# Kernel tuning notes

Hardware: AMD Instinct MI355X
Metric: run time of the kernel (lower is better)

The kernel has to match this reference:

```python
import jax, jax.numpy as jnp
import numpy as np

B, N, H, S, C = 32, 64, 128, 100, 16
SIGMA = 0.5  # perturbations.perturbed default noise scale


def setup_inputs() -> dict:
    key = jax.random.key(0)
    ks = jax.random.split(key, 8)
    x = jax.random.normal(ks[0], (B, N, H), jnp.float32)
    a = (jax.random.uniform(ks[1], (B, N, N)) < 0.1).astype(jnp.float32)
    adj = jnp.maximum(a, jnp.swapaxes(a, -1, -2))  # symmetric binary adjacency
    counts = jax.random.randint(ks[2], (B,), N // 2, N + 1)
    mask = jnp.arange(N)[None, :] < counts[:, None]
    sc = 1.0 / np.sqrt(H).astype(np.float32)
    W1 = jax.random.normal(ks[3], (H, H), jnp.float32) * sc
    b1 = jnp.zeros((H,), jnp.float32)
    W2 = jax.random.normal(ks[4], (H, H), jnp.float32) * sc
    b2 = jnp.zeros((H,), jnp.float32)
    cW1 = jax.random.normal(ks[5], (H, H), jnp.float32) * sc
    cb1 = jnp.zeros((H,), jnp.float32)
    cW2 = jax.random.normal(ks[6], (H, C), jnp.float32) * sc
    cb2 = jnp.zeros((C,), jnp.float32)
    noise = jax.random.normal(ks[7], (S * B, N, H), jnp.float32)
    return dict(x=x, adj=adj, mask=mask, W1=W1, b1=b1, W2=W2, b2=b2,
                cW1=cW1, cb1=cb1, cW2=cW2, cb2=cb2, noise=noise, num_samples=S)


def _gcn(x, adj, mask, W, b):
    # DenseGCNConv: set diag to 1, symmetric-normalize, propagate, mask.
    h = x @ W
    n = adj.shape[-1]
    eye = jnp.eye(n, dtype=bool)
    a = jnp.where(eye, 1.0, adj)
    d = jnp.clip(a.sum(-1), 1.0, None) ** -0.5
    a = d[..., :, None] * a * d[..., None, :]
    out = a @ h + b
    return out * mask[..., None].astype(out.dtype)


def _perturbed_clustering(x_all, adj_all, mask_all, cW1, cb1, cW2, cb2):
    BS, n, h = x_all.shape
    # concept MLP + argmax
    logits = jax.nn.relu(x_all @ cW1 + cb1) @ cW2 + cb2
    concepts = jnp.argmax(logits, axis=-1)  # [BS, n]
    same = concepts[:, :, None] == concepts[:, None, :]
    adj_c = jnp.where(same, adj_all, 0.0)
    # connected components via min-label propagation (scipy-order relabel)
    edge = (adj_c > 0) & mask_all[:, :, None] & mask_all[:, None, :]
    labels0 = jnp.where(mask_all, jnp.arange(n, dtype=jnp.int32), n)

    def body(_, labels):
        neigh = jnp.min(jnp.where(edge, labels[:, None, :], n), axis=-1)
        return jnp.minimum(labels, neigh)

    roots = jax.lax.fori_loop(0, n, body, labels0)  # min node idx of component
    present = jnp.zeros((BS, n + 1), jnp.int32).at[
        jnp.arange(BS)[:, None], roots].max(mask_all.astype(jnp.int32))
    rank = jnp.cumsum(present[:, :n], axis=-1)  # 1-based compact id per root
    assignments = jnp.where(
        mask_all,
        jnp.take_along_axis(rank, jnp.minimum(roots, n - 1), axis=-1), 0)
    # scatter-reduce pooling; segment ids flatten (batch, cluster); slot 0 = masked
    seg = (jnp.arange(BS, dtype=jnp.int32)[:, None] * (n + 1) + assignments).reshape(-1)
    x_new = jax.ops.segment_sum(x_all.reshape(BS * n, h), seg,
                                num_segments=BS * (n + 1)).reshape(BS, n + 1, h)[:, 1:]
    row = jax.ops.segment_max(adj_all.reshape(BS * n, n), seg,
                              num_segments=BS * (n + 1)).reshape(BS, n + 1, n)[:, 1:]
    row = jnp.maximum(row, 0.0)  # torch_scatter max includes zero-init
    colsrc = jnp.swapaxes(row, 1, 2).reshape(BS * n, n)
    adj_new = jax.ops.segment_max(colsrc, seg,
                                  num_segments=BS * (n + 1)).reshape(BS, n + 1, n)[:, 1:]
    adj_new = jnp.maximum(jnp.swapaxes(adj_new, 1, 2), 0.0)
    num_clusters = jnp.max(assignments, axis=-1)
    mask_new = jnp.arange(n)[None, :] < num_clusters[:, None]
    return x_new, adj_new, mask_new, assignments


def reference(x, adj, mask, W1, b1, W2, b2, cW1, cb1, cW2, cb2, noise, num_samples):
    # embedding GCN stack
    xe = jax.nn.relu(_gcn(x, adj, mask, W1, b1))
    x_emb = jax.nn.relu(_gcn(xe, adj, mask, W2, b2))
    Bb, n, h = x_emb.shape
    # perturbed replication (sample-major layout, matching final reshape(S, -1, ...))
    adj_all = jnp.tile(adj, (num_samples, 1, 1))
    mask_all = jnp.tile(mask, (num_samples, 1))
    x_all = jnp.tile(x_emb, (num_samples, 1, 1)) + SIGMA * noise
    x_new, adj_new, mask_new, assignments = _perturbed_clustering(
        x_all, adj_all, mask_all, cW1, cb1, cW2, cb2)
    # perturbed expectation for x_new; explicit mean/max in forward for adj/mask
    x_new = x_new.reshape(num_samples, Bb, n, h).mean(axis=0)
    adj_new = adj_new.reshape(num_samples, Bb, n, n).mean(axis=0)
    mask_new = jnp.max(mask_new.reshape(num_samples, Bb, n), axis=0)
    return x_new, adj_new, assignments, x_emb, mask_new
```

## Files before the change

kernel.cpp:

```cpp
#include <hip/hip_runtime.h>
#include <cstdint>

#define B_ 32
#define N_ 64
#define H_ 128
#define S_ 100
#define C_ 16
#define SIGMA_ 0.5f

#define OFF_XNEW 0
#define OFF_ADJN 262144
#define OFF_ASGN 393216
#define OFF_XEMB 598016
#define OFF_MSKN 860160

__device__ __forceinline__ int read_mask_elem(const void* mp, int idx) {
    const unsigned int* u = (const unsigned int*)mp;
    const unsigned int w0 = u[0], w1 = u[1];
    if (w0 == 1u) {
        if (w1 == 1u) return ((const int*)mp)[idx] != 0;
        return ((const int*)mp)[2 * idx] != 0;
    }
    if (w0 == 0x3f800000u) return ((const float*)mp)[idx] != 0.0f;
    if (w0 == 0u) return ((const double*)mp)[idx] != 0.0;
    return ((const unsigned char*)mp)[idx] != 0;
}

__global__ __launch_bounds__(256) void gcn_kernel(
    const float* __restrict__ x, const float* __restrict__ adj,
    const void* __restrict__ maskp,
    const float* __restrict__ W1, const float* __restrict__ b1,
    const float* __restrict__ W2, const float* __restrict__ b2,
    float* __restrict__ out,
    unsigned long long* __restrict__ abits_ws,
    unsigned long long* __restrict__ mbits_ws)
{
    const int b = blockIdx.x;
    const int t = threadIdx.x;
    __shared__ float Xs[N_][130];
    __shared__ float Hs[N_][130];
    __shared__ float An[N_][65];
    __shared__ float dsh[N_];
    __shared__ unsigned long long mb_sh;

    if (t < 64) {
        const int mv = read_mask_elem(maskp, b * N_ + t);
        const unsigned long long bal = __ballot(mv != 0);
        if (t == 0) { mb_sh = bal; mbits_ws[b] = bal; }
    }
    for (int row = (t >> 6); row < N_; row += 4) {
        const int j = t & 63;
        const float v = adj[((size_t)b * N_ + row) * N_ + j];
        const unsigned long long bal = __ballot(v > 0.0f);
        if (j == 0) abits_ws[b * N_ + row] = bal;
        An[row][j] = (row == j) ? 1.0f : v;
    }
    __syncthreads();
    if (t < 64) {
        float s = 0.0f;
        for (int j = 0; j < N_; ++j) s += An[t][j];
        if (s < 1.0f) s = 1.0f;
        dsh[t] = 1.0f / sqrtf(s);
    }
    __syncthreads();
    for (int e = t; e < N_ * N_; e += 256) {
        const int i = e >> 6, j = e & 63;
        An[i][j] *= dsh[i] * dsh[j];
    }
    for (int e = t; e < N_ * H_; e += 256)
        Xs[e >> 7][e & 127] = x[(size_t)b * N_ * H_ + e];
    __syncthreads();

    const int ng = t & 15, kg = t >> 4;
    const unsigned long long mb = mb_sh;

    {
        float acc[4][8] = {};
        for (int d = 0; d < H_; ++d) {
            float xv[4];
#pragma unroll
            for (int r = 0; r < 4; ++r) xv[r] = Xs[4 * ng + r][d];
            const float4 wa = *(const float4*)(W1 + d * H_ + 8 * kg);
            const float4 wb = *(const float4*)(W1 + d * H_ + 8 * kg + 4);
            const float wf[8] = {wa.x, wa.y, wa.z, wa.w, wb.x, wb.y, wb.z, wb.w};
#pragma unroll
            for (int j = 0; j < 8; ++j)
#pragma unroll
                for (int r = 0; r < 4; ++r) acc[r][j] += xv[r] * wf[j];
        }
#pragma unroll
        for (int r = 0; r < 4; ++r)
#pragma unroll
            for (int j = 0; j < 8; ++j) Hs[4 * ng + r][8 * kg + j] = acc[r][j];
    }
    __syncthreads();
    {
        float acc[4][8] = {};
        for (int j2 = 0; j2 < N_; ++j2) {
            float av[4];
#pragma unroll
            for (int r = 0; r < 4; ++r) av[r] = An[4 * ng + r][j2];
            float hv[8];
#pragma unroll
            for (int j = 0; j < 8; ++j) hv[j] = Hs[j2][8 * kg + j];
#pragma unroll
            for (int j = 0; j < 8; ++j)
#pragma unroll
                for (int r = 0; r < 4; ++r) acc[r][j] += av[r] * hv[j];
        }
        const float4 ba = *(const float4*)(b1 + 8 * kg);
        const float4 bb = *(const float4*)(b1 + 8 * kg + 4);
        const float bf[8] = {ba.x, ba.y, ba.z, ba.w, bb.x, bb.y, bb.z, bb.w};
#pragma unroll
        for (int r = 0; r < 4; ++r) {
            const int i = 4 * ng + r;
            const float m = ((mb >> i) & 1ull) ? 1.0f : 0.0f;
#pragma unroll
            for (int j = 0; j < 8; ++j)
                Xs[i][8 * kg + j] = fmaxf(acc[r][j] + bf[j], 0.0f) * m;
        }
    }
    __syncthreads();
    {
        float acc[4][8] = {};
        for (int d = 0; d < H_; ++d) {
            float xv[4];
#pragma unroll
            for (int r = 0; r < 4; ++r) xv[r] = Xs[4 * ng + r][d];
            const float4 wa = *(const float4*)(W2 + d * H_ + 8 * kg);
            const float4 wb = *(const float4*)(W2 + d * H_ + 8 * kg + 4);
            const float wf[8] = {wa.x, wa.y, wa.z, wa.w, wb.x, wb.y, wb.z, wb.w};
#pragma unroll
            for (int j = 0; j < 8; ++j)
#pragma unroll
                for (int r = 0; r < 4; ++r) acc[r][j] += xv[r] * wf[j];
        }
        __syncthreads();
#pragma unroll
        for (int r = 0; r < 4; ++r)
#pragma unroll
            for (int j = 0; j < 8; ++j) Hs[4 * ng + r][8 * kg + j] = acc[r][j];
    }
    __syncthreads();
    {
        float acc[4][8] = {};
        for (int j2 = 0; j2 < N_; ++j2) {
            float av[4];
#pragma unroll
            for (int r = 0; r < 4; ++r) av[r] = An[4 * ng + r][j2];
            float hv[8];
#pragma unroll
            for (int j = 0; j < 8; ++j) hv[j] = Hs[j2][8 * kg + j];
#pragma unroll
            for (int j = 0; j < 8; ++j)
#pragma unroll
                for (int r = 0; r < 4; ++r) acc[r][j] += av[r] * hv[j];
        }
        const float4 ba = *(const float4*)(b2 + 8 * kg);
        const float4 bb = *(const float4*)(b2 + 8 * kg + 4);
        const float bf[8] = {ba.x, ba.y, ba.z, ba.w, bb.x, bb.y, bb.z, bb.w};
#pragma unroll
        for (int r = 0; r < 4; ++r) {
            const int i = 4 * ng + r;
            const float m = ((mb >> i) & 1ull) ? 1.0f : 0.0f;
#pragma unroll
            for (int j = 0; j < 8; ++j)
                out[OFF_XEMB + (size_t)b * N_ * H_ + i * H_ + 8 * kg + j] =
                    fmaxf(acc[r][j] + bf[j], 0.0f) * m;
        }
    }
}

__device__ __forceinline__ float rscat16(float* v, int kg) {
#pragma unroll
    for (int i = 0; i < 8; ++i) {
        const float send = (kg & 8) ? v[i] : v[i + 8];
        const float recv = __shfl_xor(send, 8);
        v[i] = ((kg & 8) ? v[i + 8] : v[i]) + recv;
    }
#pragma unroll
    for (int i = 0; i < 4; ++i) {
        const float send = (kg & 4) ? v[i] : v[i + 4];
        const float recv = __shfl_xor(send, 4);
        v[i] = ((kg & 4) ? v[i + 4] : v[i]) + recv;
    }
#pragma unroll
    for (int i = 0; i < 2; ++i) {
        const float send = (kg & 2) ? v[i] : v[i + 2];
        const float recv = __shfl_xor(send, 2);
        v[i] = ((kg & 2) ? v[i + 2] : v[i]) + recv;
    }
    {
        const float send = (kg & 1) ? v[0] : v[1];
        const float recv = __shfl_xor(send, 1);
        v[0] = ((kg & 1) ? v[1] : v[0]) + recv;
    }
    return v[0];
}

__device__ __forceinline__ void argmax16(float bv, int kg, int* dst) {
    int bi = kg;
#pragma unroll
    for (int m = 1; m <= 8; m <<= 1) {
        const float ov = __shfl_xor(bv, m);
        const int   oi = __shfl_xor(bi, m);
        if (ov > bv || (ov == bv && oi < bi)) { bv = ov; bi = oi; }
    }
    if (kg == 0) *dst = bi;
}

__global__ __launch_bounds__(256) void sample_kernel(
    const float* __restrict__ noise,
    const float* __restrict__ cW1, const float* __restrict__ cb1,
    const float* __restrict__ cW2, const float* __restrict__ cb2,
    const unsigned long long* __restrict__ abits_ws,
    const unsigned long long* __restrict__ mbits_ws,
    float* __restrict__ out, int* __restrict__ gNcl)
{
    const int sb = blockIdx.x;
    const int b  = sb & (B_ - 1);
    const int t  = threadIdx.x;
    __shared__ float xa[N_ * H_];
    __shared__ int   concepts[N_];
    __shared__ unsigned long long reachL[N_];
    __shared__ unsigned long long cmS[N_];
    __shared__ unsigned long long roS[N_];
    __shared__ unsigned long long abS[N_];
    __shared__ unsigned int presLo, presHi;

    const unsigned long long mb = mbits_ws[b];
    if (t < 64) abS[t] = abits_ws[b * N_ + t];
    if (t == 0) { presLo = 0u; presHi = 0u; }

    {
        const float4* e4 = (const float4*)(out + OFF_XEMB + (size_t)b * N_ * H_);
        const float4* n4 = (const float4*)(noise + (size_t)sb * N_ * H_);
        float4* x4 = (float4*)xa;
        for (int idx = t; idx < N_ * 32; idx += 256) {
            const int i = idx >> 5, cc = idx & 31;
            const float4 ev = e4[idx], nv = n4[idx];
            float4 v;
            v.x = ev.x + SIGMA_ * nv.x;  v.y = ev.y + SIGMA_ * nv.y;
            v.z = ev.z + SIGMA_ * nv.z;  v.w = ev.w + SIGMA_ * nv.w;
            x4[i * 32 + (cc ^ (i & 7))] = v;
        }
    }
    __syncthreads();

    const int ng = t >> 4, kg = t & 15;
    float acc[4][8] = {};
    {
        const float4* x4 = (const float4*)xa;
        const int swzb = 4 * (ng & 1);
        for (int cc = 0; cc < 32; ++cc) {
            float xv[4][4];
#pragma unroll
            for (int r = 0; r < 4; ++r) {
                const float4 tmp = x4[(4 * ng + r) * 32 + (cc ^ (swzb + r))];
                xv[r][0] = tmp.x; xv[r][1] = tmp.y; xv[r][2] = tmp.z; xv[r][3] = tmp.w;
            }
#pragma unroll
            for (int dd = 0; dd < 4; ++dd) {
                const int d = cc * 4 + dd;
                const float4 wa = *(const float4*)(cW1 + d * H_ + 8 * kg);
                const float4 wb = *(const float4*)(cW1 + d * H_ + 8 * kg + 4);
                const float wf[8] = {wa.x, wa.y, wa.z, wa.w, wb.x, wb.y, wb.z, wb.w};
#pragma unroll
                for (int j = 0; j < 8; ++j)
#pragma unroll
                    for (int r = 0; r < 4; ++r) acc[r][j] += xv[r][dd] * wf[j];
            }
        }
    }
    {
        const float4 ba = *(const float4*)(cb1 + 8 * kg);
        const float4 bb = *(const float4*)(cb1 + 8 * kg + 4);
        const float bf[8] = {ba.x, ba.y, ba.z, ba.w, bb.x, bb.y, bb.z, bb.w};
        const float cb2v = cb2[kg];
#pragma unroll
        for (int r = 0; r < 4; ++r) {
            float h[8];
#pragma unroll
            for (int j = 0; j < 8; ++j) h[j] = fmaxf(acc[r][j] + bf[j], 0.0f);
            float pl[16] = {};
#pragma unroll
            for (int j = 0; j < 8; ++j) {
                const float4* w2r = (const float4*)(cW2 + (8 * kg + j) * C_);
                const float4 w0 = w2r[0], w1 = w2r[1], w2v = w2r[2], w3 = w2r[3];
                const float wf2[16] = {w0.x, w0.y, w0.z, w0.w, w1.x, w1.y, w1.z, w1.w,
                                       w2v.x, w2v.y, w2v.z, w2v.w, w3.x, w3.y, w3.z, w3.w};
#pragma unroll
                for (int c = 0; c < C_; ++c) pl[c] += h[j] * wf2[c];
            }
            const float l = rscat16(pl, kg) + cb2v;
            argmax16(l, kg, &concepts[4 * ng + r]);
        }
    }
    __syncthreads();

    unsigned long long reach = 0ull;
    int masked_i = 0;
    if (t < 64) {
        masked_i = (int)((mb >> t) & 1ull);
        if (masked_i) {
            const int ci = concepts[t];
            unsigned long long mm = abS[t] & mb;
            unsigned long long em = 0ull;
            while (mm) {
                const int j = __builtin_ctzll(mm);
                if (concepts[j] == ci) em |= (1ull << j);
                mm &= mm - 1;
            }
            reach = em | (1ull << t);
        }
        reachL[t] = reach;
    }
    __syncthreads();
    for (;;) {
        unsigned long long r = reach;
        if (masked_i) {
            unsigned long long mm = reach & ~(1ull << t);
            while (mm) {
                const int j = __builtin_ctzll(mm);
                r |= reachL[j];
                mm &= mm - 1;
            }
        }
        const int changed = (r != reach);
        __syncthreads();
        if (t < 64) reachL[t] = r;
        reach = r;
        if (!__syncthreads_or(changed)) break;
    }
    int root = 0;
    if (masked_i) {
        root = __builtin_ctzll(reach);
        if (root < 32) atomicOr(&presLo, 1u << root);
        else           atomicOr(&presHi, 1u << (root - 32));
    }
    __syncthreads();
    const unsigned long long present =
        ((unsigned long long)presHi << 32) | (unsigned long long)presLo;
    const int ncl = __popcll(present);
    if (t < 64) {
        int a_i = 0;
        if (masked_i) {
            a_i = __popcll(present & ((1ull << root) - 1ull)) + 1;
            if (root == t) {
                cmS[a_i - 1] = reach;
                unsigned long long ro = 0ull, mm = reach;
                while (mm) { const int j = __builtin_ctzll(mm); ro |= abS[j]; mm &= mm - 1; }
                roS[a_i - 1] = ro;
            }
        }
        out[OFF_ASGN + (size_t)sb * N_ + t] = (float)a_i;
    }
    __syncthreads();

    for (int e = t; e < ncl * H_; e += 256) {
        const int c = e >> 7, d = e & 127;
        unsigned long long mm = cmS[c];
        float s = 0.0f;
        while (mm) {
            const int j = __builtin_ctzll(mm);
            s += xa[j * H_ + ((((d >> 2) ^ (j & 7)) << 2) | (d & 3))];
            mm &= mm - 1;
        }
        atomicAdd(&out[OFF_XNEW + (size_t)b * N_ * H_ + e], s);
    }
    {
        int* adjCnt = (int*)out + OFF_ADJN;
        for (int idx = t; idx < ncl * N_; idx += 256) {
            const int c1 = idx >> 6, c2 = idx & 63;
            if (c2 < ncl && (roS[c1] & cmS[c2]))
                atomicAdd(&adjCnt[b * N_ * N_ + idx], 1);
        }
    }
    if (t == 0) atomicMax(&gNcl[b], ncl);
}

__global__ __launch_bounds__(256) void finalize_kernel(
    float* __restrict__ out, const int* __restrict__ gNcl)
{
    const int idx = blockIdx.x * 256 + threadIdx.x;
    if (idx < OFF_ADJN) {
        out[idx] = out[idx] / 100.0f;
    } else if (idx < OFF_ASGN) {
        const int c = ((const int*)out)[idx];
        out[idx] = (float)c / 100.0f;
    } else {
        const int m = idx - OFF_ASGN;
        if (m < B_ * N_) {
            const int bb = m >> 6, k = m & 63;
            out[OFF_MSKN + m] = (k < gNcl[bb]) ? 1.0f : 0.0f;
        }
    }
}

extern "C" void kernel_launch(void* const* d_in, const int* in_sizes, int n_in,
                              void* d_out, int out_size, void* d_ws, size_t ws_size,
                              hipStream_t stream) {
    (void)in_sizes; (void)n_in; (void)out_size; (void)ws_size;
    const float* x    = (const float*)d_in[0];
    const float* adj  = (const float*)d_in[1];
    const void*  mskp = d_in[2];
    const float* W1   = (const float*)d_in[3];
    const float* b1   = (const float*)d_in[4];
    const float* W2   = (const float*)d_in[5];
    const float* b2   = (const float*)d_in[6];
    const float* cW1  = (const float*)d_in[7];
    const float* cb1  = (const float*)d_in[8];
    const float* cW2  = (const float*)d_in[9];
    const float* cb2  = (const float*)d_in[10];
    const float* noise = (const float*)d_in[11];
    float* out = (float*)d_out;

    int* gNcl = (int*)d_ws;
    unsigned long long* abits_ws = (unsigned long long*)((char*)d_ws + 256);
    unsigned long long* mbits_ws = (unsigned long long*)((char*)d_ws + 256 + 16384);

    hipMemsetAsync(d_out, 0, (size_t)OFF_ASGN * sizeof(float), stream);
    hipMemsetAsync(d_ws, 0, 256, stream);

    gcn_kernel<<<B_, 256, 0, stream>>>(x, adj, mskp, W1, b1, W2, b2,
                                       out, abits_ws, mbits_ws);
    sample_kernel<<<S_ * B_, 256, 0, stream>>>(noise, cW1, cb1, cW2, cb2,
                                               abits_ws, mbits_ws, out, gNcl);
    finalize_kernel<<<(OFF_ASGN + B_ * N_ + 255) / 256, 256, 0, stream>>>(out, gNcl);
}
```

Before: 528.3 us.

## Replace global atomics with per-sample partial buffers and a separate reduce kernel

Each sample block now writes its full cluster-sum tile and a per-cluster adjacency bitmask into workspace instead of doing atomicAdd into the outputs. A new reduce kernel sums the 100 samples per batch, builds the adjacency counts from the bits, and computes the mask from the per-sample cluster counts. This removes atomic contention, the output memsets and the finalize pass. In exchange it writes and reads about 100 MB of partial data and needs a large workspace, falling back to the old path when the workspace is too small.

```diff
diff --git a/kernel.cpp b/kernel.cpp
--- a/kernel.cpp
+++ b/kernel.cpp
@@ -13,6 +13,13 @@
 #define OFF_ASGN 393216
 #define OFF_XEMB 598016
 #define OFF_MSKN 860160
+
+#define WS_NCL_OFF   0
+#define WS_ABITS_OFF 16384
+#define WS_MBITS_OFF 32768
+#define WS_PART_OFF  40960
+#define WS_ADJB_OFF  104898560
+#define WS_NEED      106536960ull
 
 __device__ __forceinline__ int read_mask_elem(const void* mp, int idx) {
     const unsigned int* u = (const unsigned int*)mp;
@@ -209,13 +216,17 @@
     if (kg == 0) *dst = bi;
 }
 
+template <int USE_WS>
 __global__ __launch_bounds__(256) void sample_kernel(
     const float* __restrict__ noise,
     const float* __restrict__ cW1, const float* __restrict__ cb1,
     const float* __restrict__ cW2, const float* __restrict__ cb2,
     const unsigned long long* __restrict__ abits_ws,
     const unsigned long long* __restrict__ mbits_ws,
-    float* __restrict__ out, int* __restrict__ gNcl)
+    float* __restrict__ out,
+    float* __restrict__ partial,
+    unsigned long long* __restrict__ adjbits,
+    int* __restrict__ nclArr)
 {
     const int sb = blockIdx.x;
     const int b  = sb & (B_ - 1);
@@ -357,26 +368,88 @@
     }
     __syncthreads();
 
-    for (int e = t; e < ncl * H_; e += 256) {
-        const int c = e >> 7, d = e & 127;
-        unsigned long long mm = cmS[c];
-        float s = 0.0f;
-        while (mm) {
-            const int j = __builtin_ctzll(mm);
-            s += xa[j * H_ + ((((d >> 2) ^ (j & 7)) << 2) | (d & 3))];
-            mm &= mm - 1;
-        }
-        atomicAdd(&out[OFF_XNEW + (size_t)b * N_ * H_ + e], s);
-    }
-    {
+    if (USE_WS) {
+        float* pt = partial + (size_t)sb * (N_ * H_);
+        for (int e4 = t; e4 < N_ * 32; e4 += 256) {
+            const int c = e4 >> 5, d4 = e4 & 31;
+            float4 s = {0.f, 0.f, 0.f, 0.f};
+            if (c < ncl) {
+                unsigned long long mm = cmS[c];
+                while (mm) {
+                    const int j = __builtin_ctzll(mm);
+                    const float4 v = *(const float4*)&xa[j * H_ + ((d4 ^ (j & 7)) << 2)];
+                    s.x += v.x; s.y += v.y; s.z += v.z; s.w += v.w;
+                    mm &= mm - 1;
+                }
+            }
+            *(float4*)&pt[e4 * 4] = s;
+        }
+        if (t < 64) {
+            unsigned long long row = 0ull;
+            if (t < ncl) {
+                const unsigned long long ro = roS[t];
+                for (int c2 = 0; c2 < 64; ++c2)
+                    if (c2 < ncl && (ro & cmS[c2])) row |= (1ull << c2);
+            }
+            adjbits[(size_t)sb * 64 + t] = row;
+        }
+        if (t == 0) nclArr[sb] = ncl;
+    } else {
+        for (int e = t; e < ncl * H_; e += 256) {
+            const int c = e >> 7, d = e & 127;
+            unsigned long long mm = cmS[c];
+            float s = 0.0f;
+            while (mm) {
+                const int j = __builtin_ctzll(mm);
+                s += xa[j * H_ + ((((d >> 2) ^ (j & 7)) << 2) | (d & 3))];
+                mm &= mm - 1;
+            }
+            atomicAdd(&out[OFF_XNEW + (size_t)b * N_ * H_ + e], s);
+        }
         int* adjCnt = (int*)out + OFF_ADJN;
         for (int idx = t; idx < ncl * N_; idx += 256) {
             const int c1 = idx >> 6, c2 = idx & 63;
             if (c2 < ncl && (roS[c1] & cmS[c2]))
                 atomicAdd(&adjCnt[b * N_ * N_ + idx], 1);
         }
-    }
-    if (t == 0) atomicMax(&gNcl[b], ncl);
+        if (t == 0) atomicMax(&nclArr[b], ncl);
+    }
+}
+
+__global__ __launch_bounds__(256) void reduce_kernel(
+    const float* __restrict__ partial, const unsigned long long* __restrict__ adjbits,
+    const int* __restrict__ nclArr, float* __restrict__ out)
+{
+    const int idx = blockIdx.x * 256 + threadIdx.x;
+    if (idx < 65536) {
+        const int b = idx >> 11, rem = idx & 2047;
+        float4 s = {0.f, 0.f, 0.f, 0.f};
+        const float* p = partial + (size_t)b * (N_ * H_) + rem * 4;
+#pragma unroll 4
+        for (int s_ = 0; s_ < S_; ++s_) {
+            const float4 v = *(const float4*)(p + (size_t)s_ * (B_ * N_ * H_));
+            s.x += v.x; s.y += v.y; s.z += v.z; s.w += v.w;
+        }
+        s.x *= 0.01f; s.y *= 0.01f; s.z *= 0.01f; s.w *= 0.01f;
+        *(float4*)&out[OFF_XNEW + (size_t)b * (N_ * H_) + rem * 4] = s;
+    } else if (idx < 65536 + 131072) {
+        const int j = idx - 65536;
+        const int b = j >> 12, c1 = (j >> 6) & 63, c2 = j & 63;
+        int cnt = 0;
+#pragma unroll 4
+        for (int s_ = 0; s_ < S_; ++s_)
+            cnt += (int)((adjbits[((size_t)s_ * B_ + b) * 64 + c1] >> c2) & 1ull);
+        out[OFF_ADJN + j] = (float)cnt * 0.01f;
+    } else if (idx < 65536 + 131072 + 2048) {
+        const int m = idx - 196608;
+        const int b = m >> 6, k = m & 63;
+        int mx = 0;
+        for (int s_ = 0; s_ < S_; ++s_) {
+            const int v = nclArr[s_ * B_ + b];
+            mx = v > mx ? v : mx;
+        }
+        out[OFF_MSKN + m] = (k < mx) ? 1.0f : 0.0f;
+    }
 }
 
 __global__ __launch_bounds__(256) void finalize_kernel(
@@ -400,7 +473,7 @@
 extern "C" void kernel_launch(void* const* d_in, const int* in_sizes, int n_in,
                               void* d_out, int out_size, void* d_ws, size_t ws_size,
                               hipStream_t stream) {
-    (void)in_sizes; (void)n_in; (void)out_size; (void)ws_size;
+    (void)in_sizes; (void)n_in; (void)out_size;
     const float* x    = (const float*)d_in[0];
     const float* adj  = (const float*)d_in[1];
     const void*  mskp = d_in[2];
@@ -415,16 +488,28 @@
     const float* noise = (const float*)d_in[11];
     float* out = (float*)d_out;
 
-    int* gNcl = (int*)d_ws;
-    unsigned long long* abits_ws = (unsigned long long*)((char*)d_ws + 256);
-    unsigned long long* mbits_ws = (unsigned long long*)((char*)d_ws + 256 + 16384);
-
-    hipMemsetAsync(d_out, 0, (size_t)OFF_ASGN * sizeof(float), stream);
-    hipMemsetAsync(d_ws, 0, 256, stream);
+    int* nclArr = (int*)d_ws;
+    unsigned long long* abits_ws = (unsigned long long*)((char*)d_ws + WS_ABITS_OFF);
+    unsigned long long* mbits_ws = (unsigned long long*)((char*)d_ws + WS_MBITS_OFF);
+    float* partial = (float*)((char*)d_ws + WS_PART_OFF);
+    unsigned long long* adjbits = (unsigned long long*)((char*)d_ws + WS_ADJB_OFF);
+
+    const bool use_ws = (ws_size >= WS_NEED);
 
     gcn_kernel<<<B_, 256, 0, stream>>>(x, adj, mskp, W1, b1, W2, b2,
                                        out, abits_ws, mbits_ws);
-    sample_kernel<<<S_ * B_, 256, 0, stream>>>(noise, cW1, cb1, cW2, cb2,
-                                               abits_ws, mbits_ws, out, gNcl);
-    finalize_kernel<<<(OFF_ASGN + B_ * N_ + 255) / 256, 256, 0, stream>>>(out, gNcl);
-}
+    if (use_ws) {
+        sample_kernel<1><<<S_ * B_, 256, 0, stream>>>(noise, cW1, cb1, cW2, cb2,
+                                                      abits_ws, mbits_ws, out,
+                                                      partial, adjbits, nclArr);
+        reduce_kernel<<<(65536 + 131072 + 2048) / 256, 256, 0, stream>>>(
+            partial, adjbits, nclArr, out);
+    } else {
+        hipMemsetAsync(d_out, 0, (size_t)OFF_ASGN * sizeof(float), stream);
+        hipMemsetAsync(d_ws, 0, 256, stream);
+        sample_kernel<0><<<S_ * B_, 256, 0, stream>>>(noise, cW1, cb1, cW2, cb2,
+                                                      abits_ws, mbits_ws, out,
+                                                      partial, adjbits, nclArr);
+        finalize_kernel<<<(OFF_ASGN + B_ * N_ + 255) / 256, 256, 0, stream>>>(out, nclArr);
+    }
+}
```

Result: no change. 526.6 us (-0.3%).
